# Optimization experiments

Measured on AMD Instinct MI355X. Metric: run time of the kernel, lower is better.

## Reference

```python
import math
import jax, jax.numpy as jnp
import numpy as np

NEG = -1e10


def _rope_cos_sin(T, head_dim, dtype):
    # theta_i = 10000^(-2*(i-1)/dim), i=1..dim/2  ->  j=0..dim/2-1: 10000^(-2j/dim)
    j = jnp.arange(head_dim // 2, dtype=jnp.float32)
    inv_freq = 1.0 / (10000.0 ** (2.0 * j / head_dim))
    t = jnp.arange(T, dtype=jnp.float32)
    ang = t[:, None] * inv_freq[None, :]          # [T, hd/2]
    return jnp.cos(ang).astype(dtype), jnp.sin(ang).astype(dtype)


def _apply_rope(x, cos, sin):
    # x: [B, H, T, hd]; complex multiply (cos + i sin) * (x0 + i x1)
    B, H, T, hd = x.shape
    xr = x.reshape(B, H, T, hd // 2, 2)
    x0, x1 = xr[..., 0], xr[..., 1]
    c = cos[None, None]  # [1,1,T,hd/2]
    s = sin[None, None]
    o0 = c * x0 - s * x1
    o1 = s * x0 + c * x1
    return jnp.stack([o0, o1], axis=-1).reshape(B, H, T, hd)


def setup_inputs() -> dict:
    key = jax.random.key(0)
    ks = jax.random.split(key, 9)
    B, T, C = 2, 2048, 1024
    std = 0.02
    return {
        "x": jax.random.normal(ks[0], (B, T, C), jnp.float32),
        "Wq": jax.random.normal(ks[1], (C, C), jnp.float32) * std,
        "bq": jnp.zeros((C,), jnp.float32),
        "Wk": jax.random.normal(ks[2], (C, C), jnp.float32) * std,
        "bk": jnp.zeros((C,), jnp.float32),
        "Wv": jax.random.normal(ks[3], (C, C), jnp.float32) * std,
        "bv": jnp.zeros((C,), jnp.float32),
        "Wp": jax.random.normal(ks[4], (C, C), jnp.float32) * std,
        "bp": jnp.zeros((C,), jnp.float32),
    }


def reference(x, Wq, bq, Wk, bk, Wv, bv, Wp, bp):
    B, T, C = x.shape
    H = 16
    hd = C // H

    def heads(y):  # [B,T,C] -> [B,H,T,hd]
        return y.reshape(B, T, H, hd).transpose(0, 2, 1, 3)

    q = heads(x @ Wq.T + bq)
    k = heads(x @ Wk.T + bk)
    v = heads(x @ Wv.T + bv)

    cos, sin = _rope_cos_sin(T, hd, x.dtype)
    q = _apply_rope(q, cos, sin)
    k = _apply_rope(k, cos, sin)

    att = jnp.einsum('bhqd,bhkd->bhqk', q, k) * (1.0 / math.sqrt(hd))
    causal = jnp.tril(jnp.ones((T, T), bool))
    att = jnp.where(causal[None, None], att, jnp.asarray(NEG, att.dtype))
    att = jax.nn.softmax(att, axis=-1)

    y = jnp.einsum('bhqk,bhkd->bhqd', att, v)
    y = y.transpose(0, 2, 1, 3).reshape(B, T, C)
    return y @ Wp.T + bp
```

## Files before the change

### kernel.cpp

```cpp
#include <hip/hip_runtime.h>
#include <math.h>

typedef unsigned short u16;
typedef unsigned int u32;
typedef unsigned long long u64;
typedef __attribute__((ext_vector_type(8))) short short8;
typedef __attribute__((ext_vector_type(4))) float f32x4;
typedef __attribute__((ext_vector_type(4))) u16 u16x4;
typedef __attribute__((ext_vector_type(4))) u32 u32x4;

#define AS1 __attribute__((address_space(1)))
#define AS3 __attribute__((address_space(3)))

#define QSCALE 0.18033688011112042f

__device__ __forceinline__ u16 f2bf(float f) {
  union { float f; u32 i; } u; u.f = f;
  u32 r = u.i + 0x7FFFu + ((u.i >> 16) & 1u);
  return (u16)(r >> 16);
}

__device__ __forceinline__ u32 pk_bf16(float a, float b) {
  u32 r;
  asm volatile("v_cvt_pk_bf16_f32 %0, %1, %2" : "=v"(r) : "v"(a), "v"(b));
  return r;
}

__device__ __forceinline__ void gl_lds16(const void* g, void* l) {
  __builtin_amdgcn_global_load_lds((const AS1 u32*)g, (AS3 u32*)l, 16, 0, 0);
}

#define MFMA32(a, b, c) __builtin_amdgcn_mfma_f32_16x16x32_bf16(a, b, c, 0, 0, 0)

__global__ void rope_table(float* __restrict__ cosT, float* __restrict__ sinT, int T) {
  int i = blockIdx.x * 256 + threadIdx.x;
  if (i >= T * 32) return;
  int t = i >> 5, j = i & 31;
  float inv = powf(10000.0f, -(float)j / 32.0f);
  float ang = (float)t * inv;
  cosT[i] = cosf(ang);
  sinT[i] = sinf(ang);
}

__global__ void cvt_all(const float* __restrict__ x,
                        const float* __restrict__ Wq, const float* __restrict__ Wk,
                        const float* __restrict__ Wv, const float* __restrict__ Wp,
                        u16* __restrict__ xb,
                        u16* __restrict__ Wqb, u16* __restrict__ Wkb,
                        u16* __restrict__ Wvb, u16* __restrict__ Wpb,
                        int n4x) {
  int i = blockIdx.x * 256 + threadIdx.x;
  const float* src; u16* dst; int off;
  if (i < n4x) { src = x; dst = xb; off = i; }
  else {
    int wi = i - n4x;
    int sel = wi >> 18;
    off = wi & ((1 << 18) - 1);
    src = sel == 0 ? Wq : sel == 1 ? Wk : sel == 2 ? Wv : Wp;
    dst = sel == 0 ? Wqb : sel == 1 ? Wkb : sel == 2 ? Wvb : Wpb;
  }
  float4 v = ((const float4*)src)[off];
  u16x4 o = { f2bf(v.x), f2bf(v.y), f2bf(v.z), f2bf(v.w) };
  ((u16x4*)dst)[off] = o;
}

__global__ __launch_bounds__(256, 2) void gemm_qkv(
    const u16* __restrict__ xb,
    const u16* __restrict__ Wqb, const u16* __restrict__ Wkb, const u16* __restrict__ Wvb,
    const float* __restrict__ bq, const float* __restrict__ bk, const float* __restrict__ bv,
    const float* __restrict__ cosT, const float* __restrict__ sinT,
    u16* __restrict__ Qb, u16* __restrict__ Kb, u16* __restrict__ Vb) {
  const int K = 1024, N = 1024;
  __shared__ __attribute__((aligned(16))) u16 As[128 * 32];
  __shared__ __attribute__((aligned(16))) u16 Bs[128 * 32];
  const int tid = threadIdx.x;
  const int lane = tid & 63;
  const int hi = lane >> 4, cc = lane & 15;
  const int w = tid >> 6, wm = w >> 1, wn = w & 1;
  const int sel = blockIdx.x >> 3;
  const int row0 = blockIdx.y * 128, col0 = (blockIdx.x & 7) * 128;
  const u16* W = sel == 0 ? Wqb : sel == 1 ? Wkb : Wvb;
  const float* bias = sel == 0 ? bq : sel == 1 ? bk : bv;
  u16* Out = sel == 0 ? Qb : sel == 1 ? Kb : Vb;

  const int lr = tid >> 2;
  const int lk = (tid & 3) * 8;
  const u16* Ag0 = xb + (size_t)(row0 + lr) * K + lk;
  const u16* Ag1 = xb + (size_t)(row0 + 64 + lr) * K + lk;
  const u16* Wg0 = W + (size_t)(col0 + lr) * K + lk;
  const u16* Wg1 = W + (size_t)(col0 + 64 + lr) * K + lk;
  u16* Al0 = As + tid * 8;
  u16* Al1 = As + 2048 + tid * 8;
  u16* Bl0 = Bs + tid * 8;
  u16* Bl1 = Bs + 2048 + tid * 8;

  f32x4 acc[4][4];
#pragma unroll
  for (int m = 0; m < 4; ++m)
#pragma unroll
    for (int n = 0; n < 4; ++n) acc[m][n] = f32x4{0.f, 0.f, 0.f, 0.f};

  for (int k0 = 0; k0 < K; k0 += 32) {
    __syncthreads();
    gl_lds16(Ag0 + k0, Al0);
    gl_lds16(Ag1 + k0, Al1);
    gl_lds16(Wg0 + k0, Bl0);
    gl_lds16(Wg1 + k0, Bl1);
    __syncthreads();
    short8 a[4], b[4];
#pragma unroll
    for (int m = 0; m < 4; ++m)
      a[m] = *(const short8*)(As + (wm * 64 + m * 16 + cc) * 32 + hi * 8);
#pragma unroll
    for (int n = 0; n < 4; ++n)
      b[n] = *(const short8*)(Bs + (wn * 64 + n * 16 + cc) * 32 + hi * 8);
#pragma unroll
    for (int m = 0; m < 4; ++m)
#pragma unroll
      for (int n = 0; n < 4; ++n)
        acc[m][n] = MFMA32(a[m], b[n], acc[m][n]);
  }

  if (sel < 2) {
    const float qs = (sel == 0) ? QSCALE : 1.0f;
#pragma unroll
    for (int n = 0; n < 4; ++n) {
      const int col = col0 + wn * 64 + n * 16 + cc;
      const int j = (col & 63) >> 1;
      const float bb = bias[col];
#pragma unroll
      for (int m = 0; m < 4; ++m) {
        const int rw = row0 + wm * 64 + m * 16 + hi * 4;
#pragma unroll
        for (int r = 0; r < 4; ++r) {
          const int row = rw + r;
          const int t = row & 2047;
          float v = acc[m][n][r] + bb;
          float pv = __shfl_xor(v, 1);
          float c = cosT[t * 32 + j], s = sinT[t * 32 + j];
          float oo = (cc & 1) ? (s * pv + c * v) : (c * v - s * pv);
          Out[(size_t)row * N + col] = f2bf(oo * qs);
        }
      }
    }
  } else {
#pragma unroll
    for (int n = 0; n < 4; ++n) {
      const int col = col0 + wn * 64 + n * 16 + cc;
      const float bb = bias[col];
#pragma unroll
      for (int m = 0; m < 4; ++m) {
        const int rw = row0 + wm * 64 + m * 16 + hi * 4;
#pragma unroll
        for (int r = 0; r < 4; ++r)
          Out[(size_t)(rw + r) * N + col] = f2bf(acc[m][n][r] + bb);
      }
    }
  }
}

__global__ __launch_bounds__(256, 3) void flash_mfma(
    const u16* __restrict__ Qb, const u16* __restrict__ Kb,
    const u16* __restrict__ Vb, u16* __restrict__ Yb) {
  const int T = 2048, C = 1024;
  __shared__ __attribute__((aligned(16))) u16 Ks[2][64 * 64];
  __shared__ __attribute__((aligned(16))) u16 Vt[2][64 * 64];
  __shared__ __attribute__((aligned(16))) u16 Ps[4][16 * 64];

  const int tid = threadIdx.x;
  const int lane = tid & 63;
  const int hi = lane >> 4, cc = lane & 15;
  const int hi4 = hi * 4;
  const int w = tid >> 6;
  const int qtA = blockIdx.x;
  const int qtB = 31 - qtA;
  const int bh = blockIdx.y;
  const size_t hbase = (size_t)(bh >> 4) * T * C + (size_t)(bh & 15) * 64;
  const int qA0w = qtA * 64 + w * 16;
  const int qB0w = qtB * 64 + w * 16;

  short8 qaA0, qaA1, qaB0, qaB1;
  {
    const u16* qp = Qb + hbase + (size_t)(qA0w + cc) * C + hi * 8;
    qaA0 = *(const short8*)qp;
    qaA1 = *(const short8*)(qp + 32);
    qp = Qb + hbase + (size_t)(qB0w + cc) * C + hi * 8;
    qaB0 = *(const short8*)qp;
    qaB1 = *(const short8*)(qp + 32);
  }

  f32x4 oA[4], oB[4];
#pragma unroll
  for (int nt = 0; nt < 4; ++nt) {
    oA[nt] = f32x4{0.f, 0.f, 0.f, 0.f};
    oB[nt] = f32x4{0.f, 0.f, 0.f, 0.f};
  }
  float mA = -1e30f, lA = 0.f, mB = -1e30f, lB = 0.f;

  const int krow = tid >> 2, kcol = (tid & 3) * 16;
  const int vd0 = (tid & 31) * 2, vkey0 = (tid >> 5) * 8;
  const u16* kgp = Kb + hbase + (size_t)krow * C + kcol;
  const u16* vgp = Vb + hbase + (size_t)vkey0 * C + vd0;

  short8 kr0, kr1;
  u32 vr_[8];

  auto LOADT = [&](int kt) {
    const size_t off = (size_t)(kt * 64) * C;
    kr0 = *(const short8*)(kgp + off);
    kr1 = *(const short8*)(kgp + off + 8);
#pragma unroll
    for (int j = 0; j < 8; ++j)
      vr_[j] = *(const u32*)(vgp + off + (size_t)j * C);
  };

  char* PsB = (char*)(Ps[w]);
  char* KsCur;
  char* VtCur;

  auto WRITET = [&](int buf) {
    char* KsB = (char*)(Ks[buf]);
    char* VtB = (char*)(Vt[buf]);
    const int kb = krow * 128 + kcol * 2;
    const int ksw = (krow & 7) << 4;
    *(short8*)(KsB + (kb ^ ksw)) = kr0;
    *(short8*)(KsB + ((kb + 16) ^ ksw)) = kr1;
    u32 lo0 = (vr_[0] & 0xFFFFu) | (vr_[1] << 16);
    u32 lo1 = (vr_[2] & 0xFFFFu) | (vr_[3] << 16);
    u32 lo2 = (vr_[4] & 0xFFFFu) | (vr_[5] << 16);
    u32 lo3 = (vr_[6] & 0xFFFFu) | (vr_[7] << 16);
    u32 hh0 = (vr_[0] >> 16) | (vr_[1] & 0xFFFF0000u);
    u32 hh1 = (vr_[2] >> 16) | (vr_[3] & 0xFFFF0000u);
    u32 hh2 = (vr_[4] >> 16) | (vr_[5] & 0xFFFF0000u);
    u32 hh3 = (vr_[6] >> 16) | (vr_[7] & 0xFFFF0000u);
    const int d1 = vd0 + 1;
    u32x4 vlo = {lo0, lo1, lo2, lo3};
    u32x4 vhi = {hh0, hh1, hh2, hh3};
    *(u32x4*)(VtB + ((vd0 * 128 + vkey0 * 2) ^ ((vd0 & 7) << 4))) = vlo;
    *(u32x4*)(VtB + ((d1 * 128 + vkey0 * 2) ^ ((d1 & 7) << 4))) = vhi;
  };

  const int ksw2 = (cc & 7) << 4;
  short8 kf[4][2];

  auto CHUNK = [&](const short8& qa0, const short8& qa1, f32x4* o,
                   float& mrow, float& lsum, bool diag) {
    f32x4 s[4];
#pragma unroll
    for (int nt = 0; nt < 4; ++nt) {
      f32x4 z = f32x4{0.f, 0.f, 0.f, 0.f};
      z = MFMA32(kf[nt][0], qa0, z);
      z = MFMA32(kf[nt][1], qa1, z);
      s[nt] = z;
    }
    if (diag) {
      const int qloc = w * 16 + cc;
#pragma unroll
      for (int nt = 0; nt < 4; ++nt)
#pragma unroll
        for (int r = 0; r < 4; ++r)
          if (nt * 16 + hi4 + r > qloc) s[nt][r] = -1e30f;
    }
    float tm = s[0][0];
#pragma unroll
    for (int nt = 0; nt < 4; ++nt)
#pragma unroll
      for (int r = 0; r < 4; ++r) tm = fmaxf(tm, s[nt][r]);
    tm = fmaxf(tm, __shfl_xor(tm, 16));
    tm = fmaxf(tm, __shfl_xor(tm, 32));

    const bool need = tm > mrow + 8.0f;
    float corr = 1.0f;
    if (need) { corr = exp2f(mrow - tm); mrow = tm; }

    float psum = 0.f;
#pragma unroll
    for (int nt = 0; nt < 4; ++nt) {
      float e0 = exp2f(s[nt][0] - mrow);
      float e1 = exp2f(s[nt][1] - mrow);
      float e2 = exp2f(s[nt][2] - mrow);
      float e3 = exp2f(s[nt][3] - mrow);
      psum += (e0 + e1) + (e2 + e3);
      u32 pr[2] = { pk_bf16(e0, e1), pk_bf16(e2, e3) };
      *(u64*)(PsB + ((cc * 128 + nt * 32 + hi * 8) ^ ksw2)) = *(const u64*)pr;
    }
    psum += __shfl_xor(psum, 16);
    psum += __shfl_xor(psum, 32);
    lsum = lsum * corr + psum;
    if (__any(need)) {
#pragma unroll
      for (int nt = 0; nt < 4; ++nt) o[nt] *= corr;
    }

#pragma unroll
    for (int kc = 0; kc < 2; ++kc) {
      short8 pa = *(const short8*)(PsB + ((cc * 128 + kc * 64 + hi * 16) ^ ksw2));
#pragma unroll
      for (int nt = 0; nt < 4; ++nt) {
        short8 vb = *(const short8*)(VtCur + (((nt * 16 + cc) * 128 + kc * 64 + hi * 16) ^ ksw2));
        o[nt] = MFMA32(vb, pa, o[nt]);
      }
    }
  };

  LOADT(0);
  WRITET(0);
  LOADT(1);
  __syncthreads();

  for (int kt = 0; kt <= qtB; ++kt) {
    const int cur = kt & 1;
    if (kt < qtB) {
      WRITET(cur ^ 1);
      if (kt + 1 < qtB) LOADT(kt + 2);
    }
    KsCur = (char*)(Ks[cur]);
    VtCur = (char*)(Vt[cur]);

#pragma unroll
    for (int nt = 0; nt < 4; ++nt) {
      const int kb = (nt * 16 + cc) * 128 + hi * 16;
      kf[nt][0] = *(const short8*)(KsCur + (kb ^ ksw2));
      kf[nt][1] = *(const short8*)(KsCur + ((kb + 64) ^ ksw2));
    }

    CHUNK(qaB0, qaB1, oB, mB, lB, kt == qtB);
    if (kt <= qtA) CHUNK(qaA0, qaA1, oA, mA, lA, kt == qtA);

    if (kt < qtB) __syncthreads();
  }

  const float ivA = 1.0f / lA, ivB = 1.0f / lB;
#pragma unroll
  for (int nt = 0; nt < 4; ++nt) {
    u16x4 yA = { f2bf(oA[nt][0] * ivA), f2bf(oA[nt][1] * ivA),
                 f2bf(oA[nt][2] * ivA), f2bf(oA[nt][3] * ivA) };
    *(u16x4*)(Yb + hbase + (size_t)(qA0w + cc) * C + nt * 16 + hi4) = yA;
    u16x4 yB = { f2bf(oB[nt][0] * ivB), f2bf(oB[nt][1] * ivB),
                 f2bf(oB[nt][2] * ivB), f2bf(oB[nt][3] * ivB) };
    *(u16x4*)(Yb + hbase + (size_t)(qB0w + cc) * C + nt * 16 + hi4) = yB;
  }
}

__global__ __launch_bounds__(256, 2) void gemm_proj(
    const u16* __restrict__ A, const u16* __restrict__ W,
    const float* __restrict__ bias, float* __restrict__ Out) {
  const int K = 1024, N = 1024;
  __shared__ __attribute__((aligned(16))) u16 As[128 * 32];
  __shared__ __attribute__((aligned(16))) u16 Bs[64 * 32];
  const int tid = threadIdx.x;
  const int lane = tid & 63;
  const int hi = lane >> 4, cc = lane & 15;
  const int w = tid >> 6, wm = w >> 1, wn = w & 1;
  const int row0 = blockIdx.y * 128, col0 = blockIdx.x * 64;

  const int lr = tid >> 2;
  const int lk = (tid & 3) * 8;
  const u16* Ag0 = A + (size_t)(row0 + lr) * K + lk;
  const u16* Ag1 = A + (size_t)(row0 + 64 + lr) * K + lk;
  const u16* Wg0 = W + (size_t)(col0 + lr) * K + lk;
  u16* Al0 = As + tid * 8;
  u16* Al1 = As + 2048 + tid * 8;
  u16* Bl0 = Bs + tid * 8;

  f32x4 acc[4][2];
#pragma unroll
  for (int m = 0; m < 4; ++m)
#pragma unroll
    for (int n = 0; n < 2; ++n) acc[m][n] = f32x4{0.f, 0.f, 0.f, 0.f};

  for (int k0 = 0; k0 < K; k0 += 32) {
    __syncthreads();
    gl_lds16(Ag0 + k0, Al0);
    gl_lds16(Ag1 + k0, Al1);
    gl_lds16(Wg0 + k0, Bl0);
    __syncthreads();
    short8 a[4], b[2];
#pragma unroll
    for (int m = 0; m < 4; ++m)
      a[m] = *(const short8*)(As + (wm * 64 + m * 16 + cc) * 32 + hi * 8);
#pragma unroll
    for (int n = 0; n < 2; ++n)
      b[n] = *(const short8*)(Bs + (wn * 32 + n * 16 + cc) * 32 + hi * 8);
#pragma unroll
    for (int m = 0; m < 4; ++m)
#pragma unroll
      for (int n = 0; n < 2; ++n)
        acc[m][n] = MFMA32(a[m], b[n], acc[m][n]);
  }

#pragma unroll
  for (int n = 0; n < 2; ++n) {
    const int col = col0 + wn * 32 + n * 16 + cc;
    const float bb = bias[col];
#pragma unroll
    for (int m = 0; m < 4; ++m) {
      const int rw = row0 + wm * 64 + m * 16 + hi * 4;
#pragma unroll
      for (int r = 0; r < 4; ++r)
        Out[(size_t)(rw + r) * N + col] = acc[m][n][r] + bb;
    }
  }
}

extern "C" void kernel_launch(void* const* d_in, const int* in_sizes, int n_in,
                              void* d_out, int out_size, void* d_ws, size_t ws_size,
                              hipStream_t stream) {
  const float* x  = (const float*)d_in[0];
  const float* Wq = (const float*)d_in[1];
  const float* bq = (const float*)d_in[2];
  const float* Wk = (const float*)d_in[3];
  const float* bk = (const float*)d_in[4];
  const float* Wv = (const float*)d_in[5];
  const float* bv = (const float*)d_in[6];
  const float* Wp = (const float*)d_in[7];
  const float* bp = (const float*)d_in[8];
  float* out = (float*)d_out;

  const int B = 2, T = 2048, C = 1024;
  const int M = B * T;
  const size_t MC = (size_t)M * C;
  const size_t CC = (size_t)C * C;

  char* p = (char*)d_ws;
  u16* xb  = (u16*)p;  p += MC * 2;
  u16* Wqb = (u16*)p;  p += CC * 2;
  u16* Wkb = (u16*)p;  p += CC * 2;
  u16* Wvb = (u16*)p;  p += CC * 2;
  u16* Wpb = (u16*)p;  p += CC * 2;
  u16* Qbb = (u16*)p;  p += MC * 2;
  u16* Kbb = (u16*)p;  p += MC * 2;
  u16* Vbb = (u16*)p;  p += MC * 2;
  float* cosT = (float*)p; p += (size_t)T * 32 * 4;
  float* sinT = (float*)p; p += (size_t)T * 32 * 4;

  rope_table<<<T * 32 / 256, 256, 0, stream>>>(cosT, sinT, T);
  const int n4x = (int)(MC / 4);
  const int n4tot = n4x + 4 * (int)(CC / 4);
  cvt_all<<<n4tot / 256, 256, 0, stream>>>(x, Wq, Wk, Wv, Wp, xb, Wqb, Wkb, Wvb, Wpb, n4x);

  dim3 gq(24, M / 128);
  gemm_qkv<<<gq, 256, 0, stream>>>(xb, Wqb, Wkb, Wvb, bq, bk, bv, cosT, sinT, Qbb, Kbb, Vbb);

  dim3 fg(16, B * 16);
  flash_mfma<<<fg, 256, 0, stream>>>(Qbb, Kbb, Vbb, xb);

  dim3 gp(C / 64, M / 128);
  gemm_proj<<<gp, 256, 0, stream>>>(xb, Wpb, bp, out);
}
```

Before: 130.1 us.

## Split flash attention key tiles across two blocks and merge partials

The flash attention grid gains a split dimension. Each block handles either the even or the odd key tiles for its paired query tiles and writes unnormalized fp32 output plus running max and sum to a workspace. A new merge kernel combines the two partials with log-sum-exp weights and writes bf16 output for the projection GEMM. The aim is to double the number of blocks and raise the occupancy target on the GPU. The cost is extra fp32 partial traffic and one more kernel launch.

```diff
diff --git a/kernel.cpp b/kernel.cpp
--- a/kernel.cpp
+++ b/kernel.cpp
@@ -8,6 +8,7 @@
 typedef __attribute__((ext_vector_type(4))) float f32x4;
 typedef __attribute__((ext_vector_type(4))) u16 u16x4;
 typedef __attribute__((ext_vector_type(4))) u32 u32x4;
+typedef __attribute__((ext_vector_type(8))) u16 u16x8;
 
 #define AS1 __attribute__((address_space(1)))
 #define AS3 __attribute__((address_space(3)))
@@ -159,9 +160,10 @@
   }
 }
 
-__global__ __launch_bounds__(256, 3) void flash_mfma(
+__global__ __launch_bounds__(256, 4) void flash_mfma(
     const u16* __restrict__ Qb, const u16* __restrict__ Kb,
-    const u16* __restrict__ Vb, u16* __restrict__ Yb) {
+    const u16* __restrict__ Vb, float* __restrict__ Opart,
+    float2* __restrict__ Mpart) {
   const int T = 2048, C = 1024;
   __shared__ __attribute__((aligned(16))) u16 Ks[2][64 * 64];
   __shared__ __attribute__((aligned(16))) u16 Vt[2][64 * 64];
@@ -174,7 +176,8 @@
   const int w = tid >> 6;
   const int qtA = blockIdx.x;
   const int qtB = 31 - qtA;
-  const int bh = blockIdx.y;
+  const int h = blockIdx.y;
+  const int bh = blockIdx.z;
   const size_t hbase = (size_t)(bh >> 4) * T * C + (size_t)(bh & 15) * 64;
   const int qA0w = qtA * 64 + w * 16;
   const int qB0w = qtB * 64 + w * 16;
@@ -303,16 +306,18 @@
     }
   };
 
-  LOADT(0);
+  LOADT(h);
   WRITET(0);
-  LOADT(1);
+  if (h + 2 <= qtB) LOADT(h + 2);
   __syncthreads();
 
-  for (int kt = 0; kt <= qtB; ++kt) {
-    const int cur = kt & 1;
-    if (kt < qtB) {
+  int idx = 0;
+  for (int kt = h; kt <= qtB; kt += 2, ++idx) {
+    const int cur = idx & 1;
+    const bool more = (kt + 2 <= qtB);
+    if (more) {
       WRITET(cur ^ 1);
-      if (kt + 1 < qtB) LOADT(kt + 2);
+      if (kt + 4 <= qtB) LOADT(kt + 4);
     }
     KsCur = (char*)(Ks[cur]);
     VtCur = (char*)(Vt[cur]);
@@ -327,19 +332,48 @@
     CHUNK(qaB0, qaB1, oB, mB, lB, kt == qtB);
     if (kt <= qtA) CHUNK(qaA0, qaA1, oA, mA, lA, kt == qtA);
 
-    if (kt < qtB) __syncthreads();
-  }
-
-  const float ivA = 1.0f / lA, ivB = 1.0f / lB;
+    if (more) __syncthreads();
+  }
+
+  float* Op = Opart + ((size_t)h * 65536 + (size_t)bh * 2048) * 64;
 #pragma unroll
   for (int nt = 0; nt < 4; ++nt) {
-    u16x4 yA = { f2bf(oA[nt][0] * ivA), f2bf(oA[nt][1] * ivA),
-                 f2bf(oA[nt][2] * ivA), f2bf(oA[nt][3] * ivA) };
-    *(u16x4*)(Yb + hbase + (size_t)(qA0w + cc) * C + nt * 16 + hi4) = yA;
-    u16x4 yB = { f2bf(oB[nt][0] * ivB), f2bf(oB[nt][1] * ivB),
-                 f2bf(oB[nt][2] * ivB), f2bf(oB[nt][3] * ivB) };
-    *(u16x4*)(Yb + hbase + (size_t)(qB0w + cc) * C + nt * 16 + hi4) = yB;
-  }
+    *(f32x4*)(Op + (size_t)(qA0w + cc) * 64 + nt * 16 + hi4) = oA[nt];
+    *(f32x4*)(Op + (size_t)(qB0w + cc) * 64 + nt * 16 + hi4) = oB[nt];
+  }
+  if (hi == 0) {
+    float2* Ml = Mpart + (size_t)h * 65536 + (size_t)bh * 2048;
+    Ml[qA0w + cc] = make_float2(mA, lA);
+    Ml[qB0w + cc] = make_float2(mB, lB);
+  }
+}
+
+__global__ void flash_merge(const float* __restrict__ Opart,
+                            const float2* __restrict__ Mpart,
+                            u16* __restrict__ Yb) {
+  const int i = blockIdx.x * 256 + threadIdx.x;
+  const int row = i >> 3;
+  const int d0 = (i & 7) * 8;
+  const float2 a = Mpart[row];
+  const float2 b = Mpart[65536 + row];
+  const float m = fmaxf(a.x, b.x);
+  const float wA = exp2f(a.x - m), wB = exp2f(b.x - m);
+  const float inv = 1.0f / (a.y * wA + b.y * wB);
+  const float* oA = Opart + (size_t)row * 64 + d0;
+  const float* oB = Opart + (size_t)(65536 + row) * 64 + d0;
+  f32x4 a0 = *(const f32x4*)oA;
+  f32x4 a1 = *(const f32x4*)(oA + 4);
+  f32x4 b0 = *(const f32x4*)oB;
+  f32x4 b1 = *(const f32x4*)(oB + 4);
+  u16x8 y;
+#pragma unroll
+  for (int r = 0; r < 4; ++r) {
+    y[r]     = f2bf((a0[r] * wA + b0[r] * wB) * inv);
+    y[r + 4] = f2bf((a1[r] * wA + b1[r] * wB) * inv);
+  }
+  const int bh = row >> 11, q = row & 2047;
+  u16* dst = Yb + (size_t)(bh >> 4) * 2048 * 1024 + (size_t)q * 1024 + (bh & 15) * 64 + d0;
+  *(u16x8*)dst = y;
 }
 
 __global__ __launch_bounds__(256, 2) void gemm_proj(
@@ -433,6 +467,8 @@
   u16* Vbb = (u16*)p;  p += MC * 2;
   float* cosT = (float*)p; p += (size_t)T * 32 * 4;
   float* sinT = (float*)p; p += (size_t)T * 32 * 4;
+  float* Opart = (float*)p; p += (size_t)2 * 65536 * 64 * 4;
+  float2* Mpart = (float2*)p; p += (size_t)2 * 65536 * 8;
 
   rope_table<<<T * 32 / 256, 256, 0, stream>>>(cosT, sinT, T);
   const int n4x = (int)(MC / 4);
@@ -442,8 +478,10 @@
   dim3 gq(24, M / 128);
   gemm_qkv<<<gq, 256, 0, stream>>>(xb, Wqb, Wkb, Wvb, bq, bk, bv, cosT, sinT, Qbb, Kbb, Vbb);
 
-  dim3 fg(16, B * 16);
-  flash_mfma<<<fg, 256, 0, stream>>>(Qbb, Kbb, Vbb, xb);
+  dim3 fg(16, 2, B * 16);
+  flash_mfma<<<fg, 256, 0, stream>>>(Qbb, Kbb, Vbb, Opart, Mpart);
+
+  flash_merge<<<524288 / 256, 256, 0, stream>>>(Opart, Mpart, xb);
 
   dim3 gp(C / 64, M / 128);
   gemm_proj<<<gp, 256, 0, stream>>>(xb, Wpb, bp, out);
```

New measurement: 176.1 us. +35.4%, slower.
